# Optimization experiments

Measured on AMD Instinct MI355X. Metric: run time of the kernel, lower is better.

Reference implementation:

```python
import jax, jax.numpy as jnp
import numpy as np

M, B, S, D, H, FF = 8, 64, 128, 512, 8, 1024  # modules, batch, seq, model dim, heads, ff


def setup_inputs() -> dict:
    key = jax.random.key(0)
    ks = jax.random.split(key, 24)
    r = lambda k, sh, s=1.0: (jax.random.normal(k, sh, dtype=jnp.float32) * s)
    return {
        'prev_state': r(ks[0], (M, B, D)),
        'prev_query': r(ks[1], (M, B, D)),
        'prev_key':   r(ks[2], (M, B, D)),
        'prev_value': r(ks[3], (M, B, D)),
        'key_in':     r(ks[4], (S, B, D)),
        'value_in':   r(ks[5], (S, B, D)),
        # per-module MHA projections (layout [in, out])
        'Wq': r(ks[6], (M, D, D), D ** -0.5), 'bq': jnp.zeros((M, D), jnp.float32),
        'Wk': r(ks[7], (M, D, D), D ** -0.5), 'bk': jnp.zeros((M, D), jnp.float32),
        'Wv': r(ks[8], (M, D, D), D ** -0.5), 'bv': jnp.zeros((M, D), jnp.float32),
        'Wo': r(ks[9], (M, D, D), D ** -0.5), 'bo': jnp.zeros((M, D), jnp.float32),
        # grouped output MLPs: g=0..3 -> query,key,value,state heads
        'W1': r(ks[10], (4, M, 2 * D, FF), (2 * D) ** -0.5), 'b1': jnp.zeros((4, M, FF), jnp.float32),
        'W2': r(ks[11], (4, M, FF, D), FF ** -0.5),          'b2': jnp.zeros((4, M, D), jnp.float32),
        # grouped gate MLPs (scalar gate per module)
        'Wg1': r(ks[12], (4, M, 2 * D, FF), (2 * D) ** -0.5), 'bg1': jnp.zeros((4, M, FF), jnp.float32),
        'Wg2': r(ks[13], (4, M, FF, 1), FF ** -0.5),          'bg2': jnp.zeros((4, M, 1), jnp.float32),
    }


def reference(prev_state, prev_query, prev_key, prev_value, key_in, value_in,
              Wq, bq, Wk, bk, Wv, bv, Wo, bo,
              W1, b1, W2, b2, Wg1, bg1, Wg2, bg2):
    hd = D // H
    # Per-module multi-head attention; query length is 1 per module.
    q = jnp.einsum('mbk,mkj->mbj', prev_query, Wq) + bq[:, None]          # [M,B,D]
    k = jnp.einsum('sbk,mkj->msbj', key_in, Wk) + bk[:, None, None]       # [M,S,B,D]
    v = jnp.einsum('sbk,mkj->msbj', value_in, Wv) + bv[:, None, None]     # [M,S,B,D]
    qh = q.reshape(M, B, H, hd)
    kh = k.reshape(M, S, B, H, hd)
    vh = v.reshape(M, S, B, H, hd)
    scores = jnp.einsum('mbhd,msbhd->mbhs', qh, kh) / np.float32(np.sqrt(hd))
    w = jax.nn.softmax(scores, axis=-1)                                   # [M,B,H,S]
    ao = jnp.einsum('mbhs,msbhd->mbhd', w, vh).reshape(M, B, D)
    attn_out = jnp.einsum('mbk,mkj->mbj', ao, Wo) + bo[:, None]           # [M,B,D]

    # fc_input; original MLPs apply ReLU before each Linear.
    x = jax.nn.relu(jnp.concatenate([attn_out, prev_state], axis=-1))     # [M,B,2D]
    h = jax.nn.relu(jnp.einsum('mbi,gmif->gmbf', x, W1) + b1[:, :, None])
    out = jnp.tanh(jax.nn.relu(jnp.einsum('gmbf,gmfd->gmbd', h, W2) + b2[:, :, None]))  # [4,M,B,D]
    hg = jax.nn.relu(jnp.einsum('mbi,gmif->gmbf', x, Wg1) + bg1[:, :, None])
    g = jax.nn.sigmoid(jnp.einsum('gmbf,gmfo->gmbo', hg, Wg2) + bg2[:, :, None])        # [4,M,B,1]

    prev = jnp.stack([prev_query, prev_key, prev_value, prev_state])      # matches g-group order
    new = g * out + (1.0 - g) * prev                                      # [4,M,B,D]
    # return new state tuple order (state, query, key, value) stacked -> [4,M,B,D]
    return jnp.stack([new[3], new[0], new[1], new[2]])
```

## Files before the change

kernel.cpp:

```cpp
#include <hip/hip_runtime.h>

#define M_ 8
#define B_ 64
#define S_ 128
#define D_ 512
#define H_ 8
#define FF_ 1024
#define HD_ 64

typedef __bf16 bf16x8 __attribute__((ext_vector_type(8)));
typedef float f32x4 __attribute__((ext_vector_type(4)));

__device__ __forceinline__ float bf2f(ushort u) {
    union { unsigned int i; float f; } x; x.i = ((unsigned int)u) << 16; return x.f;
}
__device__ __forceinline__ ushort f2bf(float f) {
    union { unsigned int i; float f; } x; x.f = f;
    unsigned int i = x.i;
    return (ushort)((i + 0x7FFFu + ((i >> 16) & 1u)) >> 16);
}
__device__ __forceinline__ void pack8(const float4 a, const float4 b, uint4* dst) {
    union { ushort u[8]; uint4 v; } t;
    t.u[0] = f2bf(a.x); t.u[1] = f2bf(a.y); t.u[2] = f2bf(a.z); t.u[3] = f2bf(a.w);
    t.u[4] = f2bf(b.x); t.u[5] = f2bf(b.y); t.u[6] = f2bf(b.z); t.u[7] = f2bf(b.w);
    *dst = t.v;
}

__device__ __forceinline__ void lds_sync() {
    __builtin_amdgcn_sched_barrier(0);
    asm volatile("s_waitcnt lgkmcnt(0)" ::: "memory");
    __builtin_amdgcn_s_barrier();
    __builtin_amdgcn_sched_barrier(0);
}

__device__ __forceinline__ void gemm64_fw(const float* __restrict__ X, int ldx,
                                          const float* __restrict__ Wc, int ldw,
                                          int K, short* Xs, short* Ws, f32x4* acc)
{
    const int tid = threadIdx.x, lane = tid & 63, wv = tid >> 6;
    const int c16 = lane & 15, koffs = (lane >> 4) * 8;
    const int xr = tid >> 2, xk = (tid & 3) * 8;
    const int wn = tid & 63, wk = (tid >> 6) * 8;

    float4 xa, xb; float wf[8];
    {
        const float* xp = X + xr * ldx + xk;
        xa = *(const float4*)xp; xb = *(const float4*)(xp + 4);
        const float* wp = Wc + wk * ldw + wn;
        #pragma unroll
        for (int j = 0; j < 8; ++j) wf[j] = wp[j * ldw];
    }
    #pragma unroll 1
    for (int k0 = 0; k0 < K; k0 += 32) {
        short* xs = Xs + ((k0 >> 5) & 1) * 2560;
        short* ws = Ws + ((k0 >> 5) & 1) * 2560;
        const int kn = (k0 + 32 < K) ? k0 + 32 : 0;
        const float* xp = X + xr * ldx + kn + xk;
        float4 nxa = *(const float4*)xp, nxb = *(const float4*)(xp + 4);
        float nwf[8];
        const float* wp = Wc + (kn + wk) * ldw + wn;
        #pragma unroll
        for (int j = 0; j < 8; ++j) nwf[j] = wp[j * ldw];
        __builtin_amdgcn_sched_barrier(0);

        pack8(xa, xb, (uint4*)&xs[xr * 40 + xk]);
        union { ushort u[8]; uint4 v; } tw;
        #pragma unroll
        for (int j = 0; j < 8; ++j) tw.u[j] = f2bf(wf[j]);
        *(uint4*)&ws[wn * 40 + wk] = tw.v;
        lds_sync();
        bf16x8 a = *(const bf16x8*)&xs[(16 * wv + c16) * 40 + koffs];
        #pragma unroll
        for (int t = 0; t < 4; ++t) {
            bf16x8 bfr = *(const bf16x8*)&ws[(16 * t + c16) * 40 + koffs];
            acc[t] = __builtin_amdgcn_mfma_f32_16x16x32_bf16(a, bfr, acc[t], 0, 0, 0);
        }
        xa = nxa; xb = nxb;
        #pragma unroll
        for (int j = 0; j < 8; ++j) wf[j] = nwf[j];
    }
}

__device__ __forceinline__ void gemm64_bw(const ushort* __restrict__ X, int ldx,
                                          const float* __restrict__ Wc, int ldw,
                                          int K, short* Xs, short* Ws, f32x4* acc)
{
    const int tid = threadIdx.x, lane = tid & 63, wv = tid >> 6;
    const int c16 = lane & 15, koffs = (lane >> 4) * 8;
    const int xr = tid >> 2, xk = (tid & 3) * 8;
    const int wn = tid & 63, wk = (tid >> 6) * 8;

    uint4 xv; float wf[8];
    {
        xv = *(const uint4*)&X[xr * ldx + xk];
        const float* wp = Wc + wk * ldw + wn;
        #pragma unroll
        for (int j = 0; j < 8; ++j) wf[j] = wp[j * ldw];
    }
    #pragma unroll 1
    for (int k0 = 0; k0 < K; k0 += 32) {
        short* xs = Xs + ((k0 >> 5) & 1) * 2560;
        short* ws = Ws + ((k0 >> 5) & 1) * 2560;
        const int kn = (k0 + 32 < K) ? k0 + 32 : 0;
        uint4 nxv = *(const uint4*)&X[xr * ldx + kn + xk];
        float nwf[8];
        const float* wp = Wc + (kn + wk) * ldw + wn;
        #pragma unroll
        for (int j = 0; j < 8; ++j) nwf[j] = wp[j * ldw];
        __builtin_amdgcn_sched_barrier(0);

        *(uint4*)&xs[xr * 40 + xk] = xv;
        union { ushort u[8]; uint4 v; } tw;
        #pragma unroll
        for (int j = 0; j < 8; ++j) tw.u[j] = f2bf(wf[j]);
        *(uint4*)&ws[wn * 40 + wk] = tw.v;
        lds_sync();
        bf16x8 a = *(const bf16x8*)&xs[(16 * wv + c16) * 40 + koffs];
        #pragma unroll
        for (int t = 0; t < 4; ++t) {
            bf16x8 bfr = *(const bf16x8*)&ws[(16 * t + c16) * 40 + koffs];
            acc[t] = __builtin_amdgcn_mfma_f32_16x16x32_bf16(a, bfr, acc[t], 0, 0, 0);
        }
        xv = nxv;
        #pragma unroll
        for (int j = 0; j < 8; ++j) wf[j] = nwf[j];
    }
}

__global__ __launch_bounds__(256) void k_qproj(const float* __restrict__ prev_query,
                                               const float* __restrict__ Wq,
                                               const float* __restrict__ bq,
                                               ushort* __restrict__ q_ws)
{
    __shared__ __align__(16) short Xs[2 * 64 * 40];
    __shared__ __align__(16) short Ws[2 * 64 * 40];
    const int cb = blockIdx.x, m = blockIdx.y;
    f32x4 acc[4] = {};
    gemm64_fw(prev_query + m * B_ * D_, D_, Wq + m * D_ * D_ + cb * 64, D_, D_, Xs, Ws, acc);
    const int lane = threadIdx.x & 63, wv = threadIdx.x >> 6;
    #pragma unroll
    for (int t = 0; t < 4; ++t)
        #pragma unroll
        for (int r = 0; r < 4; ++r) {
            int row = 16 * wv + (lane >> 4) * 4 + r;
            int col = cb * 64 + 16 * t + (lane & 15);
            q_ws[(m * B_ + row) * D_ + col] = f2bf(acc[t][r] + bq[m * D_ + col]);
        }
}

__global__ __launch_bounds__(256) void k_qtilde(const ushort* __restrict__ q_ws,
                                                const float* __restrict__ Wk,
                                                ushort* __restrict__ qt_ws)
{
    const int kb = blockIdx.x, h = blockIdx.y, m = blockIdx.z;
    __shared__ __align__(16) short As[64 * 72];
    __shared__ __align__(16) short Ws[64 * 72];
    const int tid = threadIdx.x, lane = tid & 63, wv = tid >> 6;
    {
        int r = lane, jj = wv * 16;
        const ushort* src = q_ws + (m * B_ + r) * D_ + h * HD_ + jj;
        *(uint4*)&As[r * 72 + jj]     = *(const uint4*)src;
        *(uint4*)&As[r * 72 + jj + 8] = *(const uint4*)(src + 8);
    }
    {
        int n = lane, jj = wv * 16;
        const float* src = Wk + m * D_ * D_ + (kb * 64 + n) * D_ + h * HD_ + jj;
        pack8(*(const float4*)src, *(const float4*)(src + 4), (uint4*)&Ws[n * 72 + jj]);
        pack8(*(const float4*)(src + 8), *(const float4*)(src + 12), (uint4*)&Ws[n * 72 + jj + 8]);
    }
    __syncthreads();
    const int c16 = lane & 15, koffs = (lane >> 4) * 8;
    f32x4 acc[4] = {};
    #pragma unroll
    for (int j0 = 0; j0 < 64; j0 += 32) {
        bf16x8 a = *(const bf16x8*)&As[(16 * wv + c16) * 72 + j0 + koffs];
        #pragma unroll
        for (int t = 0; t < 4; ++t) {
            bf16x8 bfr = *(const bf16x8*)&Ws[(16 * t + c16) * 72 + j0 + koffs];
            acc[t] = __builtin_amdgcn_mfma_f32_16x16x32_bf16(a, bfr, acc[t], 0, 0, 0);
        }
    }
    const int mh = m * H_ + h;
    #pragma unroll
    for (int t = 0; t < 4; ++t)
        #pragma unroll
        for (int r = 0; r < 4; ++r) {
            int row = 16 * wv + (lane >> 4) * 4 + r;
            int col = kb * 64 + 16 * t + (lane & 15);
            qt_ws[(mh * B_ + row) * D_ + col] = f2bf(acc[t][r]);
        }
}

__global__ __launch_bounds__(256) void k_attn2(const float* __restrict__ key_in,
                                               const float* __restrict__ value_in,
                                               const ushort* __restrict__ qt_ws,
                                               ushort* __restrict__ vt_ws)
{
    const int half = blockIdx.x, b = blockIdx.y;
    const int mh0 = half * 32;
    __shared__ __align__(16) short As[2 * 32 * 40];
    __shared__ __align__(16) short Ks[2 * 128 * 40];
    __shared__ __align__(16) short Vs[512 * 40];
    __shared__ float scs[32 * 132];
    __shared__ __align__(16) short wbuf[32 * 136];
    const int tid = threadIdx.x, lane = tid & 63, wv = tid >> 6;
    const int c16 = lane & 15, koffs = (lane >> 4) * 8;
    const int wr = wv >> 1, wc = wv & 1;
    const int BD = B_ * D_;

    f32x4 acc[4] = {};
    const int ar = tid >> 3, ak = (tid & 7) * 4;
    const int ksr = tid >> 1, kkk = (tid & 1) * 16;
    uint2 av; float4 kv0, kv1, kv2, kv3;
    {
        av = *(const uint2*)&qt_ws[((mh0 + ar) * B_ + b) * D_ + ak];
        const float* src = key_in + ksr * BD + b * D_ + kkk;
        kv0 = *(const float4*)src;       kv1 = *(const float4*)(src + 4);
        kv2 = *(const float4*)(src + 8); kv3 = *(const float4*)(src + 12);
    }
    #pragma unroll 1
    for (int k0 = 0; k0 < D_; k0 += 32) {
        short* as_ = As + ((k0 >> 5) & 1) * (32 * 40);
        short* ks_ = Ks + ((k0 >> 5) & 1) * (128 * 40);
        const int kn = (k0 + 32 < D_) ? k0 + 32 : 0;
        uint2 nav = *(const uint2*)&qt_ws[((mh0 + ar) * B_ + b) * D_ + kn + ak];
        const float* src = key_in + ksr * BD + b * D_ + kn + kkk;
        float4 nk0 = *(const float4*)src,       nk1 = *(const float4*)(src + 4);
        float4 nk2 = *(const float4*)(src + 8), nk3 = *(const float4*)(src + 12);
        __builtin_amdgcn_sched_barrier(0);

        *(uint2*)&as_[ar * 40 + ak] = av;
        pack8(kv0, kv1, (uint4*)&ks_[ksr * 40 + kkk]);
        pack8(kv2, kv3, (uint4*)&ks_[ksr * 40 + kkk + 8]);
        lds_sync();
        bf16x8 a = *(const bf16x8*)&as_[(16 * wr + c16) * 40 + koffs];
        #pragma unroll
        for (int t = 0; t < 4; ++t) {
            bf16x8 kf = *(const bf16x8*)&ks_[(64 * wc + 16 * t + c16) * 40 + koffs];
            acc[t] = __builtin_amdgcn_mfma_f32_16x16x32_bf16(a, kf, acc[t], 0, 0, 0);
        }
        av = nav; kv0 = nk0; kv1 = nk1; kv2 = nk2; kv3 = nk3;
    }
    #pragma unroll
    for (int t = 0; t < 4; ++t)
        #pragma unroll
        for (int r = 0; r < 4; ++r) {
            int row = 16 * wr + (lane >> 4) * 4 + r;
            int col = 64 * wc + 16 * t + c16;
            scs[row * 132 + col] = acc[t][r] * 0.125f;
        }
    __syncthreads();

    {
        int row = tid >> 3, sub = tid & 7;
        float mx = -1e30f;
        #pragma unroll
        for (int i = 0; i < 16; ++i) mx = fmaxf(mx, scs[row * 132 + sub + 8 * i]);
        mx = fmaxf(mx, __shfl_xor(mx, 1));
        mx = fmaxf(mx, __shfl_xor(mx, 2));
        mx = fmaxf(mx, __shfl_xor(mx, 4));
        float e[16], sm = 0.f;
        #pragma unroll
        for (int i = 0; i < 16; ++i) { e[i] = __expf(scs[row * 132 + sub + 8 * i] - mx); sm += e[i]; }
        sm += __shfl_xor(sm, 1);
        sm += __shfl_xor(sm, 2);
        sm += __shfl_xor(sm, 4);
        float rinv = 1.0f / sm;
        #pragma unroll
        for (int i = 0; i < 16; ++i)
            wbuf[row * 136 + sub + 8 * i] = (short)f2bf(e[i] * rinv);
    }
    __syncthreads();

    f32x4 vacc[16] = {};
    const int hi = tid >> 6;
    #pragma unroll 1
    for (int s0 = 0; s0 < S_; s0 += 32) {
        #pragma unroll
        for (int c = 0; c < 8; ++c) {
            int n = lane + 64 * c;
            union { ushort u[8]; uint4 v; } tv;
            #pragma unroll
            for (int j = 0; j < 8; ++j)
                tv.u[j] = f2bf(value_in[(s0 + hi * 8 + j) * BD + b * D_ + n]);
            *(uint4*)&Vs[n * 40 + hi * 8] = tv.v;
        }
        __syncthreads();
        bf16x8 a = *(const bf16x8*)&wbuf[(16 * wr + c16) * 136 + s0 + koffs];
        #pragma unroll
        for (int t = 0; t < 16; ++t) {
            bf16x8 vf = *(const bf16x8*)&Vs[(256 * wc + 16 * t + c16) * 40 + koffs];
            vacc[t] = __builtin_amdgcn_mfma_f32_16x16x32_bf16(a, vf, vacc[t], 0, 0, 0);
        }
        __syncthreads();
    }
    #pragma unroll
    for (int t = 0; t < 16; ++t)
        #pragma unroll
        for (int r = 0; r < 4; ++r) {
            int row = 16 * wr + (lane >> 4) * 4 + r;
            int col = 256 * wc + 16 * t + c16;
            vt_ws[((mh0 + row) * B_ + b) * D_ + col] = f2bf(vacc[t][r]);
        }
}

__global__ __launch_bounds__(256) void k_aoproj(const ushort* __restrict__ vt_ws,
                                                const float* __restrict__ Wv,
                                                const float* __restrict__ bv,
                                                ushort* __restrict__ ao_ws)
{
    __shared__ __align__(16) short Xs[2 * 64 * 40];
    __shared__ __align__(16) short Ws[2 * 64 * 40];
    const int h = blockIdx.x, m = blockIdx.y;
    const int mh = m * H_ + h;
    f32x4 acc[4] = {};
    gemm64_bw(vt_ws + mh * B_ * D_, D_, Wv + m * D_ * D_ + h * HD_, D_, D_, Xs, Ws, acc);
    const int lane = threadIdx.x & 63, wv = threadIdx.x >> 6;
    #pragma unroll
    for (int t = 0; t < 4; ++t)
        #pragma unroll
        for (int r = 0; r < 4; ++r) {
            int row = 16 * wv + (lane >> 4) * 4 + r;
            int col = 16 * t + (lane & 15);
            ao_ws[(m * B_ + row) * D_ + h * HD_ + col] =
                f2bf(acc[t][r] + bv[m * D_ + h * HD_ + col]);
        }
}

__global__ __launch_bounds__(256) void k_oproj(const ushort* __restrict__ ao_ws,
                                               const float* __restrict__ Wo,
                                               const float* __restrict__ bo,
                                               const float* __restrict__ prev_state,
                                               ushort* __restrict__ x_ws)
{
    __shared__ __align__(16) short Xs[2 * 64 * 40];
    __shared__ __align__(16) short Ws[2 * 64 * 40];
    const int cb = blockIdx.x, m = blockIdx.y;
    #pragma unroll
    for (int e = 0; e < 2; ++e) {
        int idx = threadIdx.x + e * 256;
        int row = idx >> 3, koff = (idx & 7) * 8;
        const float* pp = prev_state + (m * B_ + row) * D_ + cb * 64 + koff;
        float4 a = *(const float4*)pp, b = *(const float4*)(pp + 4);
        a.x = fmaxf(a.x, 0.f); a.y = fmaxf(a.y, 0.f); a.z = fmaxf(a.z, 0.f); a.w = fmaxf(a.w, 0.f);
        b.x = fmaxf(b.x, 0.f); b.y = fmaxf(b.y, 0.f); b.z = fmaxf(b.z, 0.f); b.w = fmaxf(b.w, 0.f);
        pack8(a, b, (uint4*)&x_ws[(m * B_ + row) * (2 * D_) + D_ + cb * 64 + koff]);
    }
    f32x4 acc[4] = {};
    gemm64_bw(ao_ws + m * B_ * D_, D_, Wo + m * D_ * D_ + cb * 64, D_, D_, Xs, Ws, acc);
    const int lane = threadIdx.x & 63, wv = threadIdx.x >> 6;
    #pragma unroll
    for (int t = 0; t < 4; ++t)
        #pragma unroll
        for (int r = 0; r < 4; ++r) {
            int row = 16 * wv + (lane >> 4) * 4 + r;
            int col = cb * 64 + 16 * t + (lane & 15);
            float v = fmaxf(acc[t][r] + bo[m * D_ + col], 0.0f);
            x_ws[(m * B_ + row) * (2 * D_) + col] = f2bf(v);
        }
}

__global__ __launch_bounds__(256) void k_mlp1(const ushort* __restrict__ x_ws,
                                              const float* __restrict__ W1,
                                              const float* __restrict__ b1,
                                              const float* __restrict__ Wg1,
                                              const float* __restrict__ bg1,
                                              ushort* __restrict__ h_ws,
                                              ushort* __restrict__ hg_ws)
{
    __shared__ __align__(16) short Xs[2 * 64 * 40];
    __shared__ __align__(16) short Wa[2 * 64 * 40];
    __shared__ __align__(16) short Wb[2 * 64 * 40];
    const int cb = blockIdx.x, m = blockIdx.y, g = blockIdx.z;
    const int gm = g * M_ + m;
    const float* WA = W1 + gm * 2 * D_ * FF_ + cb * 64;
    const float* WB = Wg1 + gm * 2 * D_ * FF_ + cb * 64;
    const ushort* X = x_ws + m * B_ * 2 * D_;
    const int tid = threadIdx.x, lane = tid & 63, wv = tid >> 6;
    const int c16 = lane & 15, koffs = (lane >> 4) * 8;
    const int xr = tid >> 2, xk = (tid & 3) * 8;
    const int wn = tid & 63, wk = (tid >> 6) * 8;
    f32x4 acc1[4] = {}, acc2[4] = {};

    uint4 xv; float w1f[8], w2f[8];
    {
        xv = *(const uint4*)&X[xr * (2 * D_) + xk];
        const float* wp1 = WA + wk * FF_ + wn;
        const float* wp2 = WB + wk * FF_ + wn;
        #pragma unroll
        for (int j = 0; j < 8; ++j) { w1f[j] = wp1[j * FF_]; w2f[j] = wp2[j * FF_]; }
    }
    #pragma unroll 1
    for (int k0 = 0; k0 < 2 * D_; k0 += 32) {
        short* xs = Xs + ((k0 >> 5) & 1) * 2560;
        short* wa = Wa + ((k0 >> 5) & 1) * 2560;
        short* wb = Wb + ((k0 >> 5) & 1) * 2560;
        const int kn = (k0 + 32 < 2 * D_) ? k0 + 32 : 0;
        uint4 nxv = *(const uint4*)&X[xr * (2 * D_) + kn + xk];
        float nw1[8], nw2[8];
        const float* wp1 = WA + (kn + wk) * FF_ + wn;
        const float* wp2 = WB + (kn + wk) * FF_ + wn;
        #pragma unroll
        for (int j = 0; j < 8; ++j) { nw1[j] = wp1[j * FF_]; nw2[j] = wp2[j * FF_]; }
        __builtin_amdgcn_sched_barrier(0);

        *(uint4*)&xs[xr * 40 + xk] = xv;
        union { ushort u[8]; uint4 v; } t1, t2;
        #pragma unroll
        for (int j = 0; j < 8; ++j) { t1.u[j] = f2bf(w1f[j]); t2.u[j] = f2bf(w2f[j]); }
        *(uint4*)&wa[wn * 40 + wk] = t1.v;
        *(uint4*)&wb[wn * 40 + wk] = t2.v;
        lds_sync();
        bf16x8 a = *(const bf16x8*)&xs[(16 * wv + c16) * 40 + koffs];
        #pragma unroll
        for (int t = 0; t < 4; ++t) {
            bf16x8 f1 = *(const bf16x8*)&wa[(16 * t + c16) * 40 + koffs];
            bf16x8 f2 = *(const bf16x8*)&wb[(16 * t + c16) * 40 + koffs];
            acc1[t] = __builtin_amdgcn_mfma_f32_16x16x32_bf16(a, f1, acc1[t], 0, 0, 0);
            acc2[t] = __builtin_amdgcn_mfma_f32_16x16x32_bf16(a, f2, acc2[t], 0, 0, 0);
        }
        xv = nxv;
        #pragma unroll
        for (int j = 0; j < 8; ++j) { w1f[j] = nw1[j]; w2f[j] = nw2[j]; }
    }
    #pragma unroll
    for (int t = 0; t < 4; ++t)
        #pragma unroll
        for (int r = 0; r < 4; ++r) {
            int row = 16 * wv + (lane >> 4) * 4 + r;
            int col = cb * 64 + 16 * t + c16;
            float v1 = fmaxf(acc1[t][r] + b1[gm * FF_ + col], 0.0f);
            float v2 = fmaxf(acc2[t][r] + bg1[gm * FF_ + col], 0.0f);
            h_ws [(gm * B_ + row) * FF_ + col] = f2bf(v1);
            hg_ws[(gm * B_ + row) * FF_ + col] = f2bf(v2);
        }
}

__global__ __launch_bounds__(256) void k_gate(const ushort* __restrict__ hg_ws,
                                              const float* __restrict__ Wg2,
                                              const float* __restrict__ bg2,
                                              float* __restrict__ g_ws)
{
    const int gm = blockIdx.x, bb = blockIdx.y;
    const int tid = threadIdx.x, b = bb * 8 + (tid >> 5), q = tid & 31;
    const ushort* hp = hg_ws + (gm * B_ + b) * FF_ + q * 32;
    const float* wp = Wg2 + gm * FF_ + q * 32;
    float s = 0.f;
    #pragma unroll
    for (int j = 0; j < 32; j += 8) {
        union { ushort u[8]; uint4 v; } a;
        a.v = *(const uint4*)&hp[j];
        float4 w0 = *(const float4*)&wp[j], w1 = *(const float4*)&wp[j + 4];
        s += bf2f(a.u[0]) * w0.x + bf2f(a.u[1]) * w0.y + bf2f(a.u[2]) * w0.z + bf2f(a.u[3]) * w0.w
           + bf2f(a.u[4]) * w1.x + bf2f(a.u[5]) * w1.y + bf2f(a.u[6]) * w1.z + bf2f(a.u[7]) * w1.w;
    }
    s += __shfl_xor(s, 1);
    s += __shfl_xor(s, 2);
    s += __shfl_xor(s, 4);
    s += __shfl_xor(s, 8);
    s += __shfl_xor(s, 16);
    if (q == 0)
        g_ws[gm * B_ + b] = 1.0f / (1.0f + __expf(-(s + bg2[gm])));
}

__global__ __launch_bounds__(256) void k_mlp2(const ushort* __restrict__ h_ws,
                                              const float* __restrict__ W2,
                                              const float* __restrict__ b2,
                                              const float* __restrict__ g_ws,
                                              const float* __restrict__ prev_state,
                                              const float* __restrict__ prev_query,
                                              const float* __restrict__ prev_key,
                                              const float* __restrict__ prev_value,
                                              float* __restrict__ outp)
{
    __shared__ __align__(16) short Xs[2 * 64 * 40];
    __shared__ __align__(16) short Ws[2 * 64 * 40];
    const int cb = blockIdx.x, m = blockIdx.y, g = blockIdx.z;
    const int gm = g * M_ + m;
    f32x4 acc[4] = {};
    gemm64_bw(h_ws + gm * B_ * FF_, FF_, W2 + gm * FF_ * D_ + cb * 64, D_, FF_, Xs, Ws, acc);
    const float* prev = (g == 0) ? prev_query : (g == 1) ? prev_key
                      : (g == 2) ? prev_value : prev_state;
    const int slot = (g + 1) & 3;
    const int lane = threadIdx.x & 63, wv = threadIdx.x >> 6;
    #pragma unroll
    for (int t = 0; t < 4; ++t)
        #pragma unroll
        for (int r = 0; r < 4; ++r) {
            int row = 16 * wv + (lane >> 4) * 4 + r;
            int col = cb * 64 + 16 * t + (lane & 15);
            float v = tanhf(fmaxf(acc[t][r] + b2[gm * D_ + col], 0.0f));
            float gg = g_ws[gm * B_ + row];
            float pv = prev[(m * B_ + row) * D_ + col];
            outp[((slot * M_ + m) * B_ + row) * D_ + col] = gg * v + (1.0f - gg) * pv;
        }
}

extern "C" void kernel_launch(void* const* d_in, const int* in_sizes, int n_in,
                              void* d_out, int out_size, void* d_ws, size_t ws_size,
                              hipStream_t stream)
{
    (void)in_sizes; (void)n_in; (void)out_size; (void)ws_size;
    const float* prev_state = (const float*)d_in[0];
    const float* prev_query = (const float*)d_in[1];
    const float* prev_key   = (const float*)d_in[2];
    const float* prev_value = (const float*)d_in[3];
    const float* key_in     = (const float*)d_in[4];
    const float* value_in   = (const float*)d_in[5];
    const float* Wq  = (const float*)d_in[6];
    const float* bq  = (const float*)d_in[7];
    const float* Wk  = (const float*)d_in[8];
    const float* Wv  = (const float*)d_in[10];
    const float* bv  = (const float*)d_in[11];
    const float* Wo  = (const float*)d_in[12];
    const float* bo  = (const float*)d_in[13];
    const float* W1  = (const float*)d_in[14];
    const float* b1  = (const float*)d_in[15];
    const float* W2  = (const float*)d_in[16];
    const float* b2  = (const float*)d_in[17];
    const float* Wg1 = (const float*)d_in[18];
    const float* bg1 = (const float*)d_in[19];
    const float* Wg2 = (const float*)d_in[20];
    const float* bg2 = (const float*)d_in[21];
    float* outp = (float*)d_out;

    char* ws = (char*)d_ws;
    ushort* q_ws  = (ushort*)(ws);
    ushort* ao_ws = (ushort*)(ws + (512u << 10));
    ushort* x_ws  = (ushort*)(ws + (1024u << 10));
    ushort* qt_ws = (ushort*)(ws + (2048u << 10));
    ushort* vt_ws = (ushort*)(ws + (6144u << 10));
    ushort* h_ws  = qt_ws;
    ushort* hg_ws = vt_ws;
    float*  g_ws  = (float*) (ws + (10240u << 10));

    k_qproj <<<dim3(8, 8), 256, 0, stream>>>(prev_query, Wq, bq, q_ws);
    k_qtilde<<<dim3(8, 8, 8), 256, 0, stream>>>(q_ws, Wk, qt_ws);
    k_attn2 <<<dim3(2, 64), 256, 0, stream>>>(key_in, value_in, qt_ws, vt_ws);
    k_aoproj<<<dim3(8, 8), 256, 0, stream>>>(vt_ws, Wv, bv, ao_ws);
    k_oproj <<<dim3(8, 8), 256, 0, stream>>>(ao_ws, Wo, bo, prev_state, x_ws);
    k_mlp1  <<<dim3(16, 8, 4), 256, 0, stream>>>(x_ws, W1, b1, Wg1, bg1, h_ws, hg_ws);
    k_gate  <<<dim3(32, 8), 256, 0, stream>>>(hg_ws, Wg2, bg2, g_ws);
    k_mlp2  <<<dim3(8, 8, 4), 256, 0, stream>>>(h_ws, W2, b2, g_ws,
                                                prev_state, prev_query, prev_key, prev_value, outp);
}
```

Baseline: 475.6 us.

## Split K across two warp groups in projection and MLP GEMM kernels

The 64x64-tile GEMM helpers now run with 512 threads. Two groups of four waves each process half of the K range in separate LDS buffers, and the partial accumulators are then summed through shared memory. In k_mlp1 the two groups instead handle the W1 and Wg1 products separately, sharing one X tile loaded by group 0. The aim is more waves in flight per block to hide global load latency in these small-grid kernels. The cost is an extra LDS reduction, more LDS per block, and half the threads idling in the epilogue.

```diff
diff --git a/kernel.cpp b/kernel.cpp
--- a/kernel.cpp
+++ b/kernel.cpp
@@ -33,28 +33,32 @@
     __builtin_amdgcn_sched_barrier(0);
 }
 
-__device__ __forceinline__ void gemm64_fw(const float* __restrict__ X, int ldx,
-                                          const float* __restrict__ Wc, int ldw,
-                                          int K, short* Xs, short* Ws, f32x4* acc)
-{
-    const int tid = threadIdx.x, lane = tid & 63, wv = tid >> 6;
+__device__ __forceinline__ void gemm64_fw512(const float* __restrict__ X, int ldx,
+                                             const float* __restrict__ Wc, int ldw,
+                                             int K, short* Xs, short* Ws, f32x4* acc)
+{
+    const int tid = threadIdx.x;
+    const int kg = tid >> 8, t = tid & 255;
+    const int lane = t & 63, wv = t >> 6;
     const int c16 = lane & 15, koffs = (lane >> 4) * 8;
-    const int xr = tid >> 2, xk = (tid & 3) * 8;
-    const int wn = tid & 63, wk = (tid >> 6) * 8;
-
+    const int xr = t >> 2, xk = (t & 3) * 8;
+    const int wn = t & 63, wk = (t >> 6) * 8;
+    const int K2 = K >> 1, kbase = kg * K2;
+    short* Xg = Xs + kg * 2 * 2560;
+    short* Wg = Ws + kg * 2 * 2560;
     float4 xa, xb; float wf[8];
     {
-        const float* xp = X + xr * ldx + xk;
+        const float* xp = X + xr * ldx + kbase + xk;
         xa = *(const float4*)xp; xb = *(const float4*)(xp + 4);
-        const float* wp = Wc + wk * ldw + wn;
+        const float* wp = Wc + (kbase + wk) * ldw + wn;
         #pragma unroll
         for (int j = 0; j < 8; ++j) wf[j] = wp[j * ldw];
     }
     #pragma unroll 1
-    for (int k0 = 0; k0 < K; k0 += 32) {
-        short* xs = Xs + ((k0 >> 5) & 1) * 2560;
-        short* ws = Ws + ((k0 >> 5) & 1) * 2560;
-        const int kn = (k0 + 32 < K) ? k0 + 32 : 0;
+    for (int k0 = 0; k0 < K2; k0 += 32) {
+        short* xs = Xg + ((k0 >> 5) & 1) * 2560;
+        short* ws = Wg + ((k0 >> 5) & 1) * 2560;
+        const int kn = kbase + ((k0 + 32 < K2) ? k0 + 32 : 0);
         const float* xp = X + xr * ldx + kn + xk;
         float4 nxa = *(const float4*)xp, nxb = *(const float4*)(xp + 4);
         float nwf[8];
@@ -71,37 +75,52 @@
         lds_sync();
         bf16x8 a = *(const bf16x8*)&xs[(16 * wv + c16) * 40 + koffs];
         #pragma unroll
-        for (int t = 0; t < 4; ++t) {
-            bf16x8 bfr = *(const bf16x8*)&ws[(16 * t + c16) * 40 + koffs];
-            acc[t] = __builtin_amdgcn_mfma_f32_16x16x32_bf16(a, bfr, acc[t], 0, 0, 0);
+        for (int tt = 0; tt < 4; ++tt) {
+            bf16x8 bfr = *(const bf16x8*)&ws[(16 * tt + c16) * 40 + koffs];
+            acc[tt] = __builtin_amdgcn_mfma_f32_16x16x32_bf16(a, bfr, acc[tt], 0, 0, 0);
         }
         xa = nxa; xb = nxb;
         #pragma unroll
         for (int j = 0; j < 8; ++j) wf[j] = nwf[j];
     }
-}
-
-__device__ __forceinline__ void gemm64_bw(const ushort* __restrict__ X, int ldx,
-                                          const float* __restrict__ Wc, int ldw,
-                                          int K, short* Xs, short* Ws, f32x4* acc)
-{
-    const int tid = threadIdx.x, lane = tid & 63, wv = tid >> 6;
+    __syncthreads();
+    float* red = (float*)Xs;
+    if (kg == 1) {
+        #pragma unroll
+        for (int tt = 0; tt < 4; ++tt) *(f32x4*)&red[(t * 4 + tt) * 4] = acc[tt];
+    }
+    __syncthreads();
+    if (kg == 0) {
+        #pragma unroll
+        for (int tt = 0; tt < 4; ++tt) acc[tt] += *(const f32x4*)&red[(t * 4 + tt) * 4];
+    }
+}
+
+__device__ __forceinline__ void gemm64_bw512(const ushort* __restrict__ X, int ldx,
+                                             const float* __restrict__ Wc, int ldw,
+                                             int K, short* Xs, short* Ws, f32x4* acc)
+{
+    const int tid = threadIdx.x;
+    const int kg = tid >> 8, t = tid & 255;
+    const int lane = t & 63, wv = t >> 6;
     const int c16 = lane & 15, koffs = (lane >> 4) * 8;
-    const int xr = tid >> 2, xk = (tid & 3) * 8;
-    const int wn = tid & 63, wk = (tid >> 6) * 8;
-
+    const int xr = t >> 2, xk = (t & 3) * 8;
+    const int wn = t & 63, wk = (t >> 6) * 8;
+    const int K2 = K >> 1, kbase = kg * K2;
+    short* Xg = Xs + kg * 2 * 2560;
+    short* Wg = Ws + kg * 2 * 2560;
     uint4 xv; float wf[8];
     {
-        xv = *(const uint4*)&X[xr * ldx + xk];
-        const float* wp = Wc + wk * ldw + wn;
+        xv = *(const uint4*)&X[xr * ldx + kbase + xk];
+        const float* wp = Wc + (kbase + wk) * ldw + wn;
         #pragma unroll
         for (int j = 0; j < 8; ++j) wf[j] = wp[j * ldw];
     }
     #pragma unroll 1
-    for (int k0 = 0; k0 < K; k0 += 32) {
-        short* xs = Xs + ((k0 >> 5) & 1) * 2560;
-        short* ws = Ws + ((k0 >> 5) & 1) * 2560;
-        const int kn = (k0 + 32 < K) ? k0 + 32 : 0;
+    for (int k0 = 0; k0 < K2; k0 += 32) {
+        short* xs = Xg + ((k0 >> 5) & 1) * 2560;
+        short* ws = Wg + ((k0 >> 5) & 1) * 2560;
+        const int kn = kbase + ((k0 + 32 < K2) ? k0 + 32 : 0);
         uint4 nxv = *(const uint4*)&X[xr * ldx + kn + xk];
         float nwf[8];
         const float* wp = Wc + (kn + wk) * ldw + wn;
@@ -117,35 +136,49 @@
         lds_sync();
         bf16x8 a = *(const bf16x8*)&xs[(16 * wv + c16) * 40 + koffs];
         #pragma unroll
-        for (int t = 0; t < 4; ++t) {
-            bf16x8 bfr = *(const bf16x8*)&ws[(16 * t + c16) * 40 + koffs];
-            acc[t] = __builtin_amdgcn_mfma_f32_16x16x32_bf16(a, bfr, acc[t], 0, 0, 0);
+        for (int tt = 0; tt < 4; ++tt) {
+            bf16x8 bfr = *(const bf16x8*)&ws[(16 * tt + c16) * 40 + koffs];
+            acc[tt] = __builtin_amdgcn_mfma_f32_16x16x32_bf16(a, bfr, acc[tt], 0, 0, 0);
         }
         xv = nxv;
         #pragma unroll
         for (int j = 0; j < 8; ++j) wf[j] = nwf[j];
     }
-}
-
-__global__ __launch_bounds__(256) void k_qproj(const float* __restrict__ prev_query,
-                                               const float* __restrict__ Wq,
-                                               const float* __restrict__ bq,
-                                               ushort* __restrict__ q_ws)
-{
-    __shared__ __align__(16) short Xs[2 * 64 * 40];
-    __shared__ __align__(16) short Ws[2 * 64 * 40];
+    __syncthreads();
+    float* red = (float*)Xs;
+    if (kg == 1) {
+        #pragma unroll
+        for (int tt = 0; tt < 4; ++tt) *(f32x4*)&red[(t * 4 + tt) * 4] = acc[tt];
+    }
+    __syncthreads();
+    if (kg == 0) {
+        #pragma unroll
+        for (int tt = 0; tt < 4; ++tt) acc[tt] += *(const f32x4*)&red[(t * 4 + tt) * 4];
+    }
+}
+
+__global__ __launch_bounds__(512, 4) void k_qproj(const float* __restrict__ prev_query,
+                                                  const float* __restrict__ Wq,
+                                                  const float* __restrict__ bq,
+                                                  ushort* __restrict__ q_ws)
+{
+    __shared__ __align__(16) short Xs[2 * 2 * 2560];
+    __shared__ __align__(16) short Ws[2 * 2 * 2560];
     const int cb = blockIdx.x, m = blockIdx.y;
     f32x4 acc[4] = {};
-    gemm64_fw(prev_query + m * B_ * D_, D_, Wq + m * D_ * D_ + cb * 64, D_, D_, Xs, Ws, acc);
-    const int lane = threadIdx.x & 63, wv = threadIdx.x >> 6;
-    #pragma unroll
-    for (int t = 0; t < 4; ++t)
-        #pragma unroll
-        for (int r = 0; r < 4; ++r) {
-            int row = 16 * wv + (lane >> 4) * 4 + r;
-            int col = cb * 64 + 16 * t + (lane & 15);
-            q_ws[(m * B_ + row) * D_ + col] = f2bf(acc[t][r] + bq[m * D_ + col]);
-        }
+    gemm64_fw512(prev_query + m * B_ * D_, D_, Wq + m * D_ * D_ + cb * 64, D_, D_, Xs, Ws, acc);
+    const int tid = threadIdx.x;
+    if (tid < 256) {
+        const int lane = tid & 63, wv = tid >> 6;
+        #pragma unroll
+        for (int t = 0; t < 4; ++t)
+            #pragma unroll
+            for (int r = 0; r < 4; ++r) {
+                int row = 16 * wv + (lane >> 4) * 4 + r;
+                int col = cb * 64 + 16 * t + (lane & 15);
+                q_ws[(m * B_ + row) * D_ + col] = f2bf(acc[t][r] + bq[m * D_ + col]);
+            }
+    }
 }
 
 __global__ __launch_bounds__(256) void k_qtilde(const ushort* __restrict__ q_ws,
@@ -304,41 +337,43 @@
         }
 }
 
-__global__ __launch_bounds__(256) void k_aoproj(const ushort* __restrict__ vt_ws,
-                                                const float* __restrict__ Wv,
-                                                const float* __restrict__ bv,
-                                                ushort* __restrict__ ao_ws)
-{
-    __shared__ __align__(16) short Xs[2 * 64 * 40];
-    __shared__ __align__(16) short Ws[2 * 64 * 40];
+__global__ __launch_bounds__(512, 4) void k_aoproj(const ushort* __restrict__ vt_ws,
+                                                   const float* __restrict__ Wv,
+                                                   const float* __restrict__ bv,
+                                                   ushort* __restrict__ ao_ws)
+{
+    __shared__ __align__(16) short Xs[2 * 2 * 2560];
+    __shared__ __align__(16) short Ws[2 * 2 * 2560];
     const int h = blockIdx.x, m = blockIdx.y;
     const int mh = m * H_ + h;
     f32x4 acc[4] = {};
-    gemm64_bw(vt_ws + mh * B_ * D_, D_, Wv + m * D_ * D_ + h * HD_, D_, D_, Xs, Ws, acc);
-    const int lane = threadIdx.x & 63, wv = threadIdx.x >> 6;
-    #pragma unroll
-    for (int t = 0; t < 4; ++t)
-        #pragma unroll
-        for (int r = 0; r < 4; ++r) {
-            int row = 16 * wv + (lane >> 4) * 4 + r;
-            int col = 16 * t + (lane & 15);
-            ao_ws[(m * B_ + row) * D_ + h * HD_ + col] =
-                f2bf(acc[t][r] + bv[m * D_ + h * HD_ + col]);
-        }
-}
-
-__global__ __launch_bounds__(256) void k_oproj(const ushort* __restrict__ ao_ws,
-                                               const float* __restrict__ Wo,
-                                               const float* __restrict__ bo,
-                                               const float* __restrict__ prev_state,
-                                               ushort* __restrict__ x_ws)
-{
-    __shared__ __align__(16) short Xs[2 * 64 * 40];
-    __shared__ __align__(16) short Ws[2 * 64 * 40];
+    gemm64_bw512(vt_ws + mh * B_ * D_, D_, Wv + m * D_ * D_ + h * HD_, D_, D_, Xs, Ws, acc);
+    const int tid = threadIdx.x;
+    if (tid < 256) {
+        const int lane = tid & 63, wv = tid >> 6;
+        #pragma unroll
+        for (int t = 0; t < 4; ++t)
+            #pragma unroll
+            for (int r = 0; r < 4; ++r) {
+                int row = 16 * wv + (lane >> 4) * 4 + r;
+                int col = 16 * t + (lane & 15);
+                ao_ws[(m * B_ + row) * D_ + h * HD_ + col] =
+                    f2bf(acc[t][r] + bv[m * D_ + h * HD_ + col]);
+            }
+    }
+}
+
+__global__ __launch_bounds__(512, 4) void k_oproj(const ushort* __restrict__ ao_ws,
+                                                  const float* __restrict__ Wo,
+                                                  const float* __restrict__ bo,
+                                                  const float* __restrict__ prev_state,
+                                                  ushort* __restrict__ x_ws)
+{
+    __shared__ __align__(16) short Xs[2 * 2 * 2560];
+    __shared__ __align__(16) short Ws[2 * 2 * 2560];
     const int cb = blockIdx.x, m = blockIdx.y;
-    #pragma unroll
-    for (int e = 0; e < 2; ++e) {
-        int idx = threadIdx.x + e * 256;
+    {
+        int idx = threadIdx.x;
         int row = idx >> 3, koff = (idx & 7) * 8;
         const float* pp = prev_state + (m * B_ + row) * D_ + cb * 64 + koff;
         float4 a = *(const float4*)pp, b = *(const float4*)(pp + 4);
@@ -347,92 +382,92 @@
         pack8(a, b, (uint4*)&x_ws[(m * B_ + row) * (2 * D_) + D_ + cb * 64 + koff]);
     }
     f32x4 acc[4] = {};
-    gemm64_bw(ao_ws + m * B_ * D_, D_, Wo + m * D_ * D_ + cb * 64, D_, D_, Xs, Ws, acc);
-    const int lane = threadIdx.x & 63, wv = threadIdx.x >> 6;
-    #pragma unroll
-    for (int t = 0; t < 4; ++t)
-        #pragma unroll
-        for (int r = 0; r < 4; ++r) {
-            int row = 16 * wv + (lane >> 4) * 4 + r;
-            int col = cb * 64 + 16 * t + (lane & 15);
-            float v = fmaxf(acc[t][r] + bo[m * D_ + col], 0.0f);
-            x_ws[(m * B_ + row) * (2 * D_) + col] = f2bf(v);
-        }
-}
-
-__global__ __launch_bounds__(256) void k_mlp1(const ushort* __restrict__ x_ws,
-                                              const float* __restrict__ W1,
-                                              const float* __restrict__ b1,
-                                              const float* __restrict__ Wg1,
-                                              const float* __restrict__ bg1,
-                                              ushort* __restrict__ h_ws,
-                                              ushort* __restrict__ hg_ws)
-{
-    __shared__ __align__(16) short Xs[2 * 64 * 40];
-    __shared__ __align__(16) short Wa[2 * 64 * 40];
-    __shared__ __align__(16) short Wb[2 * 64 * 40];
+    gemm64_bw512(ao_ws + m * B_ * D_, D_, Wo + m * D_ * D_ + cb * 64, D_, D_, Xs, Ws, acc);
+    const int tid = threadIdx.x;
+    if (tid < 256) {
+        const int lane = tid & 63, wv = tid >> 6;
+        #pragma unroll
+        for (int t = 0; t < 4; ++t)
+            #pragma unroll
+            for (int r = 0; r < 4; ++r) {
+                int row = 16 * wv + (lane >> 4) * 4 + r;
+                int col = cb * 64 + 16 * t + (lane & 15);
+                float v = fmaxf(acc[t][r] + bo[m * D_ + col], 0.0f);
+                x_ws[(m * B_ + row) * (2 * D_) + col] = f2bf(v);
+            }
+    }
+}
+
+__global__ __launch_bounds__(512, 4) void k_mlp1(const ushort* __restrict__ x_ws,
+                                                 const float* __restrict__ W1,
+                                                 const float* __restrict__ b1,
+                                                 const float* __restrict__ Wg1,
+                                                 const float* __restrict__ bg1,
+                                                 ushort* __restrict__ h_ws,
+                                                 ushort* __restrict__ hg_ws)
+{
+    __shared__ __align__(16) short smem[6 * 2560];
     const int cb = blockIdx.x, m = blockIdx.y, g = blockIdx.z;
     const int gm = g * M_ + m;
-    const float* WA = W1 + gm * 2 * D_ * FF_ + cb * 64;
-    const float* WB = Wg1 + gm * 2 * D_ * FF_ + cb * 64;
+    const int tid = threadIdx.x;
+    const int kg = tid >> 8, t = tid & 255;
+    const int lane = t & 63, wv = t >> 6;
+    const int c16 = lane & 15, koffs = (lane >> 4) * 8;
+    const int xr = t >> 2, xk = (t & 3) * 8;
+    const int wn = t & 63, wk = (t >> 6) * 8;
+    const float* Wm = (kg == 0 ? W1 : Wg1) + gm * 2 * D_ * FF_ + cb * 64;
     const ushort* X = x_ws + m * B_ * 2 * D_;
-    const int tid = threadIdx.x, lane = tid & 63, wv = tid >> 6;
-    const int c16 = lane & 15, koffs = (lane >> 4) * 8;
-    const int xr = tid >> 2, xk = (tid & 3) * 8;
-    const int wn = tid & 63, wk = (tid >> 6) * 8;
-    f32x4 acc1[4] = {}, acc2[4] = {};
-
-    uint4 xv; float w1f[8], w2f[8];
-    {
-        xv = *(const uint4*)&X[xr * (2 * D_) + xk];
-        const float* wp1 = WA + wk * FF_ + wn;
-        const float* wp2 = WB + wk * FF_ + wn;
-        #pragma unroll
-        for (int j = 0; j < 8; ++j) { w1f[j] = wp1[j * FF_]; w2f[j] = wp2[j * FF_]; }
+    short* Xs = smem;
+    short* Wg = smem + 2 * 2560 + kg * 2 * 2560;
+    f32x4 acc[4] = {};
+
+    uint4 xv = {};
+    float wf[8];
+    {
+        if (kg == 0) xv = *(const uint4*)&X[xr * (2 * D_) + xk];
+        const float* wp = Wm + wk * FF_ + wn;
+        #pragma unroll
+        for (int j = 0; j < 8; ++j) wf[j] = wp[j * FF_];
     }
     #pragma unroll 1
     for (int k0 = 0; k0 < 2 * D_; k0 += 32) {
         short* xs = Xs + ((k0 >> 5) & 1) * 2560;
-        short* wa = Wa + ((k0 >> 5) & 1) * 2560;
-        short* wb = Wb + ((k0 >> 5) & 1) * 2560;
+        short* ws = Wg + ((k0 >> 5) & 1) * 2560;
         const int kn = (k0 + 32 < 2 * D_) ? k0 + 32 : 0;
-        uint4 nxv = *(const uint4*)&X[xr * (2 * D_) + kn + xk];
-        float nw1[8], nw2[8];
-        const float* wp1 = WA + (kn + wk) * FF_ + wn;
-        const float* wp2 = WB + (kn + wk) * FF_ + wn;
-        #pragma unroll
-        for (int j = 0; j < 8; ++j) { nw1[j] = wp1[j * FF_]; nw2[j] = wp2[j * FF_]; }
+        uint4 nxv = {};
+        if (kg == 0) nxv = *(const uint4*)&X[xr * (2 * D_) + kn + xk];
+        float nwf[8];
+        const float* wp = Wm + (kn + wk) * FF_ + wn;
+        #pragma unroll
+        for (int j = 0; j < 8; ++j) nwf[j] = wp[j * FF_];
         __builtin_amdgcn_sched_barrier(0);
 
-        *(uint4*)&xs[xr * 40 + xk] = xv;
-        union { ushort u[8]; uint4 v; } t1, t2;
-        #pragma unroll
-        for (int j = 0; j < 8; ++j) { t1.u[j] = f2bf(w1f[j]); t2.u[j] = f2bf(w2f[j]); }
-        *(uint4*)&wa[wn * 40 + wk] = t1.v;
-        *(uint4*)&wb[wn * 40 + wk] = t2.v;
+        if (kg == 0) *(uint4*)&xs[xr * 40 + xk] = xv;
+        union { ushort u[8]; uint4 v; } tw;
+        #pragma unroll
+        for (int j = 0; j < 8; ++j) tw.u[j] = f2bf(wf[j]);
+        *(uint4*)&ws[wn * 40 + wk] = tw.v;
         lds_sync();
         bf16x8 a = *(const bf16x8*)&xs[(16 * wv + c16) * 40 + koffs];
         #pragma unroll
-        for (int t = 0; t < 4; ++t) {
-            bf16x8 f1 = *(const bf16x8*)&wa[(16 * t + c16) * 40 + koffs];
-            bf16x8 f2 = *(const bf16x8*)&wb[(16 * t + c16) * 40 + koffs];
-            acc1[t] = __builtin_amdgcn_mfma_f32_16x16x32_bf16(a, f1, acc1[t], 0, 0, 0);
-            acc2[t] = __builtin_amdgcn_mfma_f32_16x16x32_bf16(a, f2, acc2[t], 0, 0, 0);
+        for (int tt = 0; tt < 4; ++tt) {
+            bf16x8 bfr = *(const bf16x8*)&ws[(16 * tt + c16) * 40 + koffs];
+            acc[tt] = __builtin_amdgcn_mfma_f32_16x16x32_bf16(a, bfr, acc[tt], 0, 0, 0);
         }
         xv = nxv;
         #pragma unroll
-        for (int j = 0; j < 8; ++j) { w1f[j] = nw1[j]; w2f[j] = nw2[j]; }
-    }
+        for (int j = 0; j < 8; ++j) wf[j] = nwf[j];
+    }
+    const float* bias = (kg == 0) ? b1 : bg1;
+    ushort* dst = (kg == 0) ? h_ws : hg_ws;
     #pragma unroll
-    for (int t = 0; t < 4; ++t)
+    for (int tt = 0; tt < 4; ++tt)
         #pragma unroll
         for (int r = 0; r < 4; ++r) {
             int row = 16 * wv + (lane >> 4) * 4 + r;
-            int col = cb * 64 + 16 * t + c16;
-            float v1 = fmaxf(acc1[t][r] + b1[gm * FF_ + col], 0.0f);
-            float v2 = fmaxf(acc2[t][r] + bg1[gm * FF_ + col], 0.0f);
-            h_ws [(gm * B_ + row) * FF_ + col] = f2bf(v1);
-            hg_ws[(gm * B_ + row) * FF_ + col] = f2bf(v2);
+            int col = cb * 64 + 16 * tt + c16;
+            float v = fmaxf(acc[tt][r] + bias[gm * FF_ + col], 0.0f);
+            dst[(gm * B_ + row) * FF_ + col] = f2bf(v);
         }
 }
 
@@ -463,37 +498,40 @@
         g_ws[gm * B_ + b] = 1.0f / (1.0f + __expf(-(s + bg2[gm])));
 }
 
-__global__ __launch_bounds__(256) void k_mlp2(const ushort* __restrict__ h_ws,
-                                              const float* __restrict__ W2,
-                                              const float* __restrict__ b2,
-                                              const float* __restrict__ g_ws,
-                                              const float* __restrict__ prev_state,
-                                              const float* __restrict__ prev_query,
-                                              const float* __restrict__ prev_key,
-                                              const float* __restrict__ prev_value,
-                                              float* __restrict__ outp)
-{
-    __shared__ __align__(16) short Xs[2 * 64 * 40];
-    __shared__ __align__(16) short Ws[2 * 64 * 40];
+__global__ __launch_bounds__(512, 4) void k_mlp2(const ushort* __restrict__ h_ws,
+                                                 const float* __restrict__ W2,
+                                                 const float* __restrict__ b2,
+                                                 const float* __restrict__ g_ws,
+                                                 const float* __restrict__ prev_state,
+                                                 const float* __restrict__ prev_query,
+                                                 const float* __restrict__ prev_key,
+                                                 const float* __restrict__ prev_value,
+                                                 float* __restrict__ outp)
+{
+    __shared__ __align__(16) short Xs[2 * 2 * 2560];
+    __shared__ __align__(16) short Ws[2 * 2 * 2560];
     const int cb = blockIdx.x, m = blockIdx.y, g = blockIdx.z;
     const int gm = g * M_ + m;
     f32x4 acc[4] = {};
-    gemm64_bw(h_ws + gm * B_ * FF_, FF_, W2 + gm * FF_ * D_ + cb * 64, D_, FF_, Xs, Ws, acc);
+    gemm64_bw512(h_ws + gm * B_ * FF_, FF_, W2 + gm * FF_ * D_ + cb * 64, D_, FF_, Xs, Ws, acc);
     const float* prev = (g == 0) ? prev_query : (g == 1) ? prev_key
                       : (g == 2) ? prev_value : prev_state;
     const int slot = (g + 1) & 3;
-    const int lane = threadIdx.x & 63, wv = threadIdx.x >> 6;
-    #pragma unroll
-    for (int t = 0; t < 4; ++t)
-        #pragma unroll
-        for (int r = 0; r < 4; ++r) {
-            int row = 16 * wv + (lane >> 4) * 4 + r;
-            int col = cb * 64 + 16 * t + (lane & 15);
-            float v = tanhf(fmaxf(acc[t][r] + b2[gm * D_ + col], 0.0f));
-            float gg = g_ws[gm * B_ + row];
-            float pv = prev[(m * B_ + row) * D_ + col];
-            outp[((slot * M_ + m) * B_ + row) * D_ + col] = gg * v + (1.0f - gg) * pv;
-        }
+    const int tid = threadIdx.x;
+    if (tid < 256) {
+        const int lane = tid & 63, wv = tid >> 6;
+        #pragma unroll
+        for (int t = 0; t < 4; ++t)
+            #pragma unroll
+            for (int r = 0; r < 4; ++r) {
+                int row = 16 * wv + (lane >> 4) * 4 + r;
+                int col = cb * 64 + 16 * t + (lane & 15);
+                float v = tanhf(fmaxf(acc[t][r] + b2[gm * D_ + col], 0.0f));
+                float gg = g_ws[gm * B_ + row];
+                float pv = prev[(m * B_ + row) * D_ + col];
+                outp[((slot * M_ + m) * B_ + row) * D_ + col] = gg * v + (1.0f - gg) * pv;
+            }
+    }
 }
 
 extern "C" void kernel_launch(void* const* d_in, const int* in_sizes, int n_in,
@@ -534,13 +572,13 @@
     ushort* hg_ws = vt_ws;
     float*  g_ws  = (float*) (ws + (10240u << 10));
 
-    k_qproj <<<dim3(8, 8), 256, 0, stream>>>(prev_query, Wq, bq, q_ws);
+    k_qproj <<<dim3(8, 8), 512, 0, stream>>>(prev_query, Wq, bq, q_ws);
     k_qtilde<<<dim3(8, 8, 8), 256, 0, stream>>>(q_ws, Wk, qt_ws);
     k_attn2 <<<dim3(2, 64), 256, 0, stream>>>(key_in, value_in, qt_ws, vt_ws);
-    k_aoproj<<<dim3(8, 8), 256, 0, stream>>>(vt_ws, Wv, bv, ao_ws);
-    k_oproj <<<dim3(8, 8), 256, 0, stream>>>(ao_ws, Wo, bo, prev_state, x_ws);
-    k_mlp1  <<<dim3(16, 8, 4), 256, 0, stream>>>(x_ws, W1, b1, Wg1, bg1, h_ws, hg_ws);
+    k_aoproj<<<dim3(8, 8), 512, 0, stream>>>(vt_ws, Wv, bv, ao_ws);
+    k_oproj <<<dim3(8, 8), 512, 0, stream>>>(ao_ws, Wo, bo, prev_state, x_ws);
+    k_mlp1  <<<dim3(16, 8, 4), 512, 0, stream>>>(x_ws, W1, b1, Wg1, bg1, h_ws, hg_ws);
     k_gate  <<<dim3(32, 8), 256, 0, stream>>>(hg_ws, Wg2, bg2, g_ws);
-    k_mlp2  <<<dim3(8, 8, 4), 256, 0, stream>>>(h_ws, W2, b2, g_ws,
+    k_mlp2  <<<dim3(8, 8, 4), 512, 0, stream>>>(h_ws, W2, b2, g_ws,
                                                 prev_state, prev_query, prev_key, prev_value, outp);
 }
```

Result: faster. 461.9 us (-2.9%).
